# Kernel tuning notes

Measured on AMD Instinct MI355X. Metric: run time of the kernel, lower is better.

## Reference

```python
import jax, jax.numpy as jnp
import numpy as np

NUM_T = 1000      # diffusion timesteps
TIME_DIM = 16     # gaussian time embedding size
DIST_DIM = 16     # gaussian distance embedding size


def _gsmear(x, stop, num_g):
    # GaussianSmearing with linearly spaced centers in [0, stop]
    offsets = jnp.linspace(0.0, stop, num_g)
    coeff = -0.5 / (offsets[1] - offsets[0]) ** 2
    return jnp.exp(coeff * (x[:, None] - offsets[None, :]) ** 2)


def setup_inputs():
    key = jax.random.key(0)
    ks = jax.random.split(key, 20)
    N, EH, G = 20000, 100000, 1000          # nodes, halfedges, graphs
    NT, ND, ED, L, NE = 16, 256, 128, 2, 5   # node types, node_dim, edge_dim, blocks, edge types
    h_node = jax.nn.one_hot(jax.random.randint(ks[0], (N,), 0, NT), NT, dtype=jnp.float32)
    pos_node = jax.random.normal(ks[1], (N, 3), dtype=jnp.float32) * 3.0
    batch_node = jnp.sort(jax.random.randint(ks[2], (N,), 0, G))
    half = jax.random.randint(ks[3], (2, EH), 0, N)
    edge_index = jnp.concatenate([half, half[::-1]], axis=1)  # halfedges + flipped
    bh = jnp.sort(jax.random.randint(ks[4], (EH,), 0, G))
    batch_edge = jnp.concatenate([bh, bh], axis=0)
    t = jax.random.randint(ks[5], (G,), 0, NUM_T)

    def w(k, shape):
        fan_in = shape[-2] if len(shape) > 1 else shape[-1]
        return jax.random.normal(k, shape, dtype=jnp.float32) / np.sqrt(fan_in)

    e_in = ED + 2 * ND + DIST_DIM + 1
    return {
        'h_node': h_node, 'pos_node': pos_node, 'batch_node': batch_node,
        'edge_index': edge_index, 'batch_edge': batch_edge, 't': t,
        'W_node_emb': w(ks[6], (NT, ND - TIME_DIM)),
        'W_edge_emb': w(ks[7], (2 * NT, ED - TIME_DIM)),
        'We1': w(ks[8], (L, e_in, ED)), 'be1': jnp.zeros((L, ED), jnp.float32),
        'We2': w(ks[9], (L, ED, ED)), 'be2': jnp.zeros((L, ED), jnp.float32),
        'Wm': w(ks[10], (L, ND + ED, ND)), 'bm': jnp.zeros((L, ND), jnp.float32),
        'Wn1': w(ks[11], (L, 2 * ND + 1, ND)), 'bn1': jnp.zeros((L, ND), jnp.float32),
        'Wn2': w(ks[12], (L, ND, ND)), 'bn2': jnp.zeros((L, ND), jnp.float32),
        'Wd1': w(ks[13], (ED + ND, ED)), 'bd1': jnp.zeros((ED,), jnp.float32),
        'Wd2': w(ks[14], (ED, ED)), 'bd2': jnp.zeros((ED,), jnp.float32),
        'Wd3': w(ks[15], (ED, NE)), 'bd3': jnp.zeros((NE,), jnp.float32),
    }


def reference(h_node, pos_node, batch_node, edge_index, batch_edge, t,
              W_node_emb, W_edge_emb, We1, be1, We2, be2, Wm, bm,
              Wn1, bn1, Wn2, bn2, Wd1, bd1, Wd2, bd2, Wd3, bd3):
    src, dst = edge_index[0], edge_index[1]
    N = h_node.shape[0]
    L = We1.shape[0]

    # edge input features: concat of endpoint node features (gather)
    h_e0 = jnp.concatenate([h_node[src], h_node[dst]], axis=-1)

    tn = t[batch_node].astype(jnp.float32)  # per-node timestep
    te = t[batch_edge].astype(jnp.float32)  # per-edge timestep
    # linear embed + gaussian-smeared time embedding
    h_n = jnp.concatenate([h_node @ W_node_emb, _gsmear(tn, float(NUM_T), TIME_DIM)], axis=-1)
    h_e = jnp.concatenate([h_e0 @ W_edge_emb, _gsmear(te, float(NUM_T), TIME_DIM)], axis=-1)
    node_time = (tn / NUM_T)[:, None]
    edge_time = (te / NUM_T)[:, None]

    # geometric edge features
    d = jnp.linalg.norm(pos_node[dst] - pos_node[src], axis=-1)
    dist_emb = _gsmear(d, 10.0, DIST_DIM)

    # NodeEdgeNet: alternating edge / node residual updates
    for l in range(L):
        e_in = jnp.concatenate([h_e, h_n[src], h_n[dst], dist_emb, edge_time], axis=-1)
        h_e = h_e + jax.nn.relu(e_in @ We1[l] + be1[l]) @ We2[l] + be2[l]
        msg = jax.nn.relu(jnp.concatenate([h_n[src], h_e], axis=-1) @ Wm[l] + bm[l])
        agg = jax.ops.segment_sum(msg, dst, num_segments=N)
        n_in = jnp.concatenate([h_n, agg, node_time], axis=-1)
        h_n = h_n + jax.nn.relu(n_in @ Wn1[l] + bn1[l]) @ Wn2[l] + bn2[l]

    # symmetrize halfedges and decode edge types
    nh = h_e.shape[0] // 2
    h_ext = jnp.concatenate([h_e[:nh] + h_e[nh:],
                             h_n[src[:nh]] + h_n[dst[:nh]]], axis=-1)
    h = jax.nn.relu(h_ext @ Wd1 + bd1)
    h = jax.nn.relu(h @ Wd2 + bd2)
    return h @ Wd3 + bd3
```

## Files before the change

kernel.cpp:

```cpp
#include <hip/hip_runtime.h>
#include <math.h>


typedef __attribute__((ext_vector_type(8)))  short bf16x8;
typedef __attribute__((ext_vector_type(16))) float f32x16;

__device__ __forceinline__ float b2f(unsigned short u) {
    union { float f; unsigned int i; } x; x.i = ((unsigned int)u) << 16; return x.f;
}
__device__ __forceinline__ unsigned short f2b(float f) {
    union { float f; unsigned int i; } x; x.f = f;
    unsigned int r = x.i + 0x7fffu + ((x.i >> 16) & 1u);
    return (unsigned short)(r >> 16);
}
__device__ __forceinline__ bf16x8 ld8(const unsigned short* p) { return *(const bf16x8*)p; }
__device__ __forceinline__ bf16x8 zero8() { bf16x8 r = {0,0,0,0,0,0,0,0}; return r; }
__device__ __forceinline__ bf16x8 add8(bf16x8 a, bf16x8 b) {
    bf16x8 r;
#pragma unroll
    for (int j = 0; j < 8; j++) r[j] = (short)f2b(b2f((unsigned short)a[j]) + b2f((unsigned short)b[j]));
    return r;
}

#define MFMA4(ACC, A0, A1, B0, B1)                                                   \
    ACC[0][0] = __builtin_amdgcn_mfma_f32_32x32x16_bf16(A0, B0, ACC[0][0], 0, 0, 0); \
    ACC[0][1] = __builtin_amdgcn_mfma_f32_32x32x16_bf16(A0, B1, ACC[0][1], 0, 0, 0); \
    ACC[1][0] = __builtin_amdgcn_mfma_f32_32x32x16_bf16(A1, B0, ACC[1][0], 0, 0, 0); \
    ACC[1][1] = __builtin_amdgcn_mfma_f32_32x32x16_bf16(A1, B1, ACC[1][1], 0, 0, 0);

#define LANE_SETUP()                                  \
    const int tid  = threadIdx.x;                     \
    const int lane = tid & 63;                        \
    const int wave = tid >> 6;                        \
    const int wm = wave >> 1, wn = wave & 1;          \
    const int l31 = lane & 31, l5 = lane >> 5;        \
    (void)wm; (void)wn; (void)lane;

#define PIPELINE4(NITER, FETCH, ACC)                                  \
    {                                                                 \
        bf16x8 pa0[2], pb0[2], pa1[2], pb1[2], pa2[2], pb2[2];        \
        FETCH(0, pa0, pb0);                                           \
        if (1 < (NITER)) FETCH(1, pa1, pb1);                          \
        _Pragma("unroll")                                             \
        for (int i = 0; i < (NITER); i++) {                           \
            if (i + 2 < (NITER)) FETCH(i + 2, pa2, pb2);              \
            MFMA4(ACC, pa0[0], pa0[1], pb0[0], pb0[1]);               \
            pa0[0] = pa1[0]; pa0[1] = pa1[1];                         \
            pb0[0] = pb1[0]; pb0[1] = pb1[1];                         \
            pa1[0] = pa2[0]; pa1[1] = pa2[1];                         \
            pb1[0] = pb2[0]; pb1[1] = pb2[1];                         \
        }                                                             \
    }

#define PIPELINE2(NITER, FETCH, ACC)                                  \
    {                                                                 \
        bf16x8 pa0, pb0[2], pa1, pb1[2], pa2, pb2[2];                 \
        FETCH(0, pa0, pb0);                                           \
        if (1 < (NITER)) FETCH(1, pa1, pb1);                          \
        _Pragma("unroll")                                             \
        for (int i = 0; i < (NITER); i++) {                           \
            if (i + 2 < (NITER)) FETCH(i + 2, pa2, pb2);              \
            ACC[0] = __builtin_amdgcn_mfma_f32_32x32x16_bf16(pa0, pb0[0], ACC[0], 0, 0, 0); \
            ACC[1] = __builtin_amdgcn_mfma_f32_32x32x16_bf16(pa0, pb0[1], ACC[1], 0, 0, 0); \
            pa0 = pa1; pb0[0] = pb1[0]; pb0[1] = pb1[1];              \
            pa1 = pa2; pb1[0] = pb2[0]; pb1[1] = pb2[1];              \
        }                                                             \
    }

__global__ void zero_i32_k(int* p, int n) {
    int i = blockIdx.x * 256 + threadIdx.x;
    if (i < n) p[i] = 0;
}
__global__ void hist_k(const int* __restrict__ dst, int* __restrict__ cnt, int E) {
    int e = blockIdx.x * 256 + threadIdx.x;
    if (e < E) atomicAdd(&cnt[dst[e]], 1);
}
__global__ __launch_bounds__(256) void scan_k(int* __restrict__ cnt, int N) {
    __shared__ int s[256];
    const int tidx  = threadIdx.x;
    const int chunk = (N + 255) / 256;
    const int lo = tidx * chunk;
    const int hi = (lo + chunk < N) ? lo + chunk : N;
    int sum = 0;
    for (int i = lo; i < hi; i++) sum += cnt[i];
    s[tidx] = sum;
    __syncthreads();
    for (int d = 1; d < 256; d <<= 1) {
        int t = (tidx >= d) ? s[tidx - d] : 0;
        __syncthreads();
        s[tidx] += t;
        __syncthreads();
    }
    int base = s[tidx] - sum;
    for (int i = lo; i < hi; i++) {
        int c = cnt[i];
        cnt[i] = base;
        base += c;
    }
}
__global__ void fill_k(const int* __restrict__ src, const int* __restrict__ dst,
                       const int* __restrict__ batch_edge, int* __restrict__ cur,
                       int* __restrict__ eids, int* __restrict__ pos,
                       int* __restrict__ srcp, int* __restrict__ dstp,
                       int* __restrict__ bep, int E) {
    int e = blockIdx.x * 256 + threadIdx.x;
    if (e < E) {
        int p = atomicAdd(&cur[dst[e]], 1);
        eids[p] = e;
        pos[e]  = p;
        srcp[p] = src[e];
        dstp[p] = dst[e];
        bep[p]  = batch_edge[e];
    }
}
__global__ void pad_k(int* eids, int* srcp, int* dstp, int* bep, int E, int Epad) {
    int i = E + blockIdx.x * 256 + threadIdx.x;
    if (i < Epad) { eids[i] = -1; srcp[i] = 0; dstp[i] = -1; bep[i] = 0; }
}

// ... 39 lines not shown
            int col = seg * 8 + j;
            float dx = x - (1000.0f / 15.0f) * (float)(col - 240);
            v[j] = (short)f2b(expf(-1.125e-4f * dx * dx));
        }
    }
    *(bf16x8*)&h_n[(size_t)row * 256 + seg * 8] = v;
}

__global__ void embed_edge_k(const int* __restrict__ typ,
                             const float* __restrict__ We,
                             const int* __restrict__ srcp,
                             const int* __restrict__ dstp,
                             const int* __restrict__ bep,
                             const int* __restrict__ t,
                             unsigned short* __restrict__ h_e, int E) {
    int idx = blockIdx.x * 256 + threadIdx.x;
    if (idx >= E * 16) return;
    int row = idx >> 4, seg = idx & 15;
    bf16x8 v;
    if (seg < 14) {
        int d0 = dstp[row]; if (d0 < 0) d0 = 0;
        const float* ws = We + (size_t)typ[srcp[row]] * 112 + seg * 8;
        const float* wd = We + (size_t)(16 + typ[d0]) * 112 + seg * 8;
#pragma unroll
        for (int j = 0; j < 8; j++) v[j] = (short)f2b(ws[j] + wd[j]);
    } else {
        float x = (float)t[bep[row]];
#pragma unroll
        for (int j = 0; j < 8; j++) {
            int col = seg * 8 + j;
            float dx = x - (1000.0f / 15.0f) * (float)(col - 112);
            v[j] = (short)f2b(expf(-1.125e-4f * dx * dx));
        }
    }
    *(bf16x8*)&h_e[(size_t)row * 128 + seg * 8] = v;
}

__global__ __launch_bounds__(256) void edge_fused_k(
    unsigned short* __restrict__ h_e, const unsigned short* __restrict__ h_n,
    const unsigned short* __restrict__ Wt1, const float* __restrict__ be1,
    const unsigned short* __restrict__ Wt2, const float* __restrict__ be2,
    const float* __restrict__ pos, const int* __restrict__ srcp,
    const int* __restrict__ dstp, const int* __restrict__ t,
    const int* __restrict__ bep, int E)
{
    __shared__ __align__(16) char smem[128 * 136 * 2];
    unsigned short (*As)[8][8] = (unsigned short(*)[8][8])smem;
    unsigned short (*Bs)[8][8] = (unsigned short(*)[8][8])(smem + 16384);
    unsigned short (*H)[136]   = (unsigned short(*)[136])smem;

    LANE_SETUP();
    const int row0 = blockIdx.x * 128;
    const int srow = tid >> 3, sks = tid & 7;

    int rge[4], sg[4], dg[4]; bool okr[4];
#pragma unroll
    for (int p = 0; p < 4; p++) {
        int r = row0 + srow + p * 32;
        okr[p] = r < E;
        rge[p] = okr[p] ? r : 0;
        sg[p]  = srcp[rge[p]];
        dg[p]  = dstp[rge[p]]; if (dg[p] < 0) dg[p] = 0;
    }

    f32x16 acc[2][2] = {};
    for (int kc = 0; kc < 11; kc++) {
        const int cg = kc * 8 + sks;
#pragma unroll
        for (int p = 0; p < 4; p++) {
            int row = srow + p * 32;
            bf16x8 v;
            if (!okr[p] || cg >= 83) {
                v = zero8();
            } else if (cg < 16) {
                v = ld8(h_e + (size_t)rge[p] * 128 + (cg << 3));
            } else if (cg < 48) {
                v = ld8(h_n + (size_t)sg[p] * 256 + ((cg - 16) << 3));
            } else if (cg < 80) {
                v = ld8(h_n + (size_t)dg[p] * 256 + ((cg - 48) << 3));
            } else if (cg < 82) {
                float dx = pos[dg[p] * 3 + 0] - pos[sg[p] * 3 + 0];
                float dy = pos[dg[p] * 3 + 1] - pos[sg[p] * 3 + 1];
                float dz = pos[dg[p] * 3 + 2] - pos[sg[p] * 3 + 2];
                float dist = sqrtf(dx * dx + dy * dy + dz * dz);
#pragma unroll
                for (int j = 0; j < 8; j++) {
                    float u = dist - (10.0f / 15.0f) * (float)((cg - 80) * 8 + j);
                    v[j] = (short)f2b(expf(-1.125f * u * u));
                }
            } else {
                v = zero8();
                v[0] = (short)f2b((float)t[bep[rge[p]]] * 1e-3f);
            }
            *(bf16x8*)&As[row][sks ^ (row & 7)][0] = v;
        }
#pragma unroll
        for (int p = 0; p < 4; p++) {
            int col = srow + p * 32;
            bf16x8 v = (cg < 84) ? ld8(Wt1 + (size_t)col * 672 + (cg << 3)) : zero8();
            *(bf16x8*)&Bs[col][sks ^ (col & 7)][0] = v;
        }
        __syncthreads();
#pragma unroll
        for (int s = 0; s < 4; s++) {
            const int ks  = s * 2 + l5;
            const int ra0 = wm * 64 + l31, ra1 = ra0 + 32;
            const int ca0 = wn * 64 + l31, ca1 = ca0 + 32;
            bf16x8 a0 = *(const bf16x8*)&As[ra0][ks ^ (ra0 & 7)][0];
            bf16x8 a1 = *(const bf16x8*)&As[ra1][ks ^ (ra1 & 7)][0];
            bf16x8 b0 = *(const bf16x8*)&Bs[ca0][ks ^ (ca0 & 7)][0];
            bf16x8 b1 = *(const bf16x8*)&Bs[ca1][ks ^ (ca1 & 7)][0];
            MFMA4(acc, a0, a1, b0, b1);
        }
        __syncthreads();
    }

#pragma unroll
    for (int mt = 0; mt < 2; mt++)
#pragma unroll
        for (int nt = 0; nt < 2; nt++)
#pragma unroll
            for (int r = 0; r < 16; r++) {
                int lrow = wm * 64 + mt * 32 + (r & 3) + 8 * (r >> 2) + 4 * l5;
                int col  = wn * 64 + nt * 32 + l31;
                float v = acc[mt][nt][r] + be1[col];
                H[lrow][col] = f2b(fmaxf(v, 0.f));
            }
    __syncthreads();

    const unsigned short* W2a = Wt2 + (size_t)(wn * 64 + l31) * 128;
    const unsigned short* W2b = Wt2 + (size_t)(wn * 64 + 32 + l31) * 128;
    f32x16 acc2[2][2] = {};
#define EF2_FETCH(i, A, B)                                          \
    {                                                               \
        const int c = 2 * (i) + l5;                                 \
        A[0] = *(const bf16x8*)&H[wm * 64 + l31][c << 3];           \
        A[1] = *(const bf16x8*)&H[wm * 64 + 32 + l31][c << 3];      \
        B[0] = ld8(W2a + (c << 3));                                 \
        B[1] = ld8(W2b + (c << 3));                                 \
    }
    PIPELINE4(8, EF2_FETCH, acc2)
#undef EF2_FETCH

#pragma unroll
    for (int mt = 0; mt < 2; mt++)
#pragma unroll
        for (int nt = 0; nt < 2; nt++)
#pragma unroll
            for (int r = 0; r < 16; r++) {
                int lrow = wm * 64 + mt * 32 + (r & 3) + 8 * (r >> 2) + 4 * l5;
                int grow = row0 + lrow;
                if (grow >= E) continue;
                int col = wn * 64 + nt * 32 + l31;
                size_t off = (size_t)grow * 128 + col;
                float v = acc2[mt][nt][r] + be2[col] + b2f(h_e[off]);
                h_e[off] = f2b(v);
            }
}

__global__ __launch_bounds__(256) void msg_k(
    const unsigned short* __restrict__ h_e, const unsigned short* __restrict__ h_n,
    const unsigned short* __restrict__ Wtm, const float* __restrict__ bm,
    const int* __restrict__ srcp, const int* __restrict__ dstp,
    float* __restrict__ agg, int E, int nRowTiles)
{
    __shared__ __align__(16) char smem[33024 + 512];
    unsigned short (*As)[8][8] = (unsigned short(*)[8][8])smem;
    unsigned short (*Bs)[8][8] = (unsigned short(*)[8][8])(smem + 16384);
    float (*T)[129] = (float(*)[129])smem;
    int* dstv = (int*)(smem + 33024);

    LANE_SETUP();
    const int b    = blockIdx.x;
    const int rowt = (b >> 4) * 8 + (b & 7);
    const int colh = (b >> 3) & 1;
    if (rowt >= nRowTiles) return;
    const int row0 = rowt * 128;
    const int col0 = colh * 128;

    if (tid < 128) dstv[tid] = dstp[row0 + tid];

    const int srow = tid >> 3, sks = tid & 7;

    f32x16 acc[2][2] = {};
    for (int kc = 0; kc < 6; kc++) {
        const int cg = kc * 8 + sks;
#pragma unroll
        for (int p = 0; p < 4; p++) {
            int row = srow + p * 32;
            int r   = row0 + row;
            bf16x8 v;
            if (r < E) {
                if (cg < 32) v = ld8(h_n + (size_t)srcp[r] * 256 + (cg << 3));
                else         v = ld8(h_e + (size_t)r * 128 + ((cg - 32) << 3));
            } else v = zero8();
            *(bf16x8*)&As[row][sks ^ (row & 7)][0] = v;
        }
#pragma unroll
        for (int p = 0; p < 4; p++) {
            int col = srow + p * 32;
            bf16x8 v = ld8(Wtm + (size_t)(col0 + col) * 384 + (cg << 3));
            *(bf16x8*)&Bs[col][sks ^ (col & 7)][0] = v;
        }
        __syncthreads();
#pragma unroll
        for (int s = 0; s < 4; s++) {
            const int ks  = s * 2 + l5;
            const int ra0 = wm * 64 + l31, ra1 = ra0 + 32;
            const int ca0 = wn * 64 + l31, ca1 = ca0 + 32;
            bf16x8 a0 = *(const bf16x8*)&As[ra0][ks ^ (ra0 & 7)][0];
            bf16x8 a1 = *(const bf16x8*)&As[ra1][ks ^ (ra1 & 7)][0];
            bf16x8 b0 = *(const bf16x8*)&Bs[ca0][ks ^ (ca0 & 7)][0];
            bf16x8 b1 = *(const bf16x8*)&Bs[ca1][ks ^ (ca1 & 7)][0];
            MFMA4(acc, a0, a1, b0, b1);
        }
        __syncthreads();
    }

    for (int ph = 0; ph < 2; ph++) {
        __syncthreads();
        if (wm == ph) {
#pragma unroll
            for (int mt = 0; mt < 2; mt++)
#pragma unroll
                for (int nt = 0; nt < 2; nt++)
#pragma unroll
                    for (int r = 0; r < 16; r++) {
                        int lrow = mt * 32 + (r & 3) + 8 * (r >> 2) + 4 * l5;
                        int col  = wn * 64 + nt * 32 + l31;
                        T[lrow][col] = acc[mt][nt][r] + bm[col0 + col];
                    }
        }
        __syncthreads();
        const int col = tid & 127, seg = tid >> 7;
        const int gcol = col0 + col;
        float run = 0.f; int prev = -1;
#pragma unroll 4
        for (int i = 0; i < 32; i++) {
            int lr = seg * 32 + i;
            int d  = dstv[ph * 64 + lr];
            float v = fmaxf(T[lr][col], 0.f);
            if (d != prev) {
                if (prev >= 0 && run != 0.f) atomicAdd(&agg[(size_t)prev * 256 + gcol], run);
                run = 0.f; prev = d;
            }
            if (d >= 0) run += v;
        }
        if (prev >= 0 && run != 0.f) atomicAdd(&agg[(size_t)prev * 256 + gcol], run);
    }
}

__global__ __launch_bounds__(256) void nin_k(
    const unsigned short* __restrict__ h_n, const float* __restrict__ agg,
    const unsigned short* __restrict__ Wtn1, const float* __restrict__ bn1,
    const int* __restrict__ batch_node, const int* __restrict__ t,
    unsigned short* __restrict__ Hn, int N)
{
    LANE_SETUP();
    const int row0 = blockIdx.x * 64;
    const int col0 = blockIdx.y * 128;

    int rr = row0 + wm * 32 + l31;
    bool ok = rr < N;
    int r = ok ? rr : 0;
    float timev = (float)t[batch_node[r]] * 1e-3f;
    const unsigned short* hp = h_n + (size_t)r * 256;
    const float*          ap = agg + (size_t)r * 256;

    const unsigned short* Wa = Wtn1 + (size_t)(col0 + wn * 64 + l31) * 544;
    const unsigned short* Wb = Wtn1 + (size_t)(col0 + wn * 64 + 32 + l31) * 544;

    f32x16 acc[2] = {};
#define NIN_FETCH(i, A, B)                                              \
    {                                                                   \
        const int c = 2 * (i) + l5;                                     \
        if (!ok) A = zero8();                                           \
        else if (c < 32) A = ld8(hp + (c << 3));                        \
        else if (c < 64) {                                              \
            const float* q = ap + ((c - 32) << 3);                      \
            bf16x8 v;                                                   \
            _Pragma("unroll")                                           \
            for (int j = 0; j < 8; j++) v[j] = (short)f2b(q[j]);        \
            A = v;                                                      \
        } else if (c == 64) { A = zero8(); A[0] = (short)f2b(timev); }  \
        else A = zero8();                                               \
        B[0] = ld8(Wa + (c << 3));                                      \
        B[1] = ld8(Wb + (c << 3));                                      \
    }
    PIPELINE2(34, NIN_FETCH, acc)
#undef NIN_FETCH

#pragma unroll
    for (int nt = 0; nt < 2; nt++)
#pragma unroll
        for (int r2 = 0; r2 < 16; r2++) {
            int lrow = wm * 32 + (r2 & 3) + 8 * (r2 >> 2) + 4 * l5;
            int grow = row0 + lrow;
            if (grow >= N) continue;
            int col = col0 + wn * 64 + nt * 32 + l31;
            float v = fmaxf(acc[nt][r2] + bn1[col], 0.f);
            Hn[(size_t)grow * 256 + col] = f2b(v);
        }
}

__global__ __launch_bounds__(256) void node_plain_k(
    const unsigned short* __restrict__ Hn, const unsigned short* __restrict__ Wtn2,
    const float* __restrict__ bn2, unsigned short* __restrict__ h_n, int N)
{
    LANE_SETUP();
    const int row0 = blockIdx.x * 64;
    const int col0 = blockIdx.y * 128;

    int rr = row0 + wm * 32 + l31;
    bool ok = rr < N;
    const unsigned short* hp = Hn + (size_t)(ok ? rr : 0) * 256;

    const unsigned short* Wa = Wtn2 + (size_t)(col0 + wn * 64 + l31) * 256;
    const unsigned short* Wb = Wtn2 + (size_t)(col0 + wn * 64 + 32 + l31) * 256;

    f32x16 acc[2] = {};
#define NP_FETCH(i, A, B)                          \
    {                                              \
        const int c = 2 * (i) + l5;                \
        A = ok ? ld8(hp + (c << 3)) : zero8();     \
        B[0] = ld8(Wa + (c << 3));                 \
        B[1] = ld8(Wb + (c << 3));                 \
    }
    PIPELINE2(16, NP_FETCH, acc)
#undef NP_FETCH

#pragma unroll
    for (int nt = 0; nt < 2; nt++)
#pragma unroll
        for (int r2 = 0; r2 < 16; r2++) {
            int lrow = wm * 32 + (r2 & 3) + 8 * (r2 >> 2) + 4 * l5;
            int grow = row0 + lrow;
            if (grow >= N) continue;
            int col = col0 + wn * 64 + nt * 32 + l31;
            size_t off = (size_t)grow * 256 + col;
            float v = acc[nt][r2] + bn2[col] + b2f(h_n[off]);
            h_n[off] = f2b(v);
        }
}

__global__ __launch_bounds__(256) void dec_fused_k(
    const unsigned short* __restrict__ h_e, const unsigned short* __restrict__ h_n,
    const unsigned short* __restrict__ Wtd1, const float* __restrict__ bd1,
    const unsigned short* __restrict__ Wtd2, const float* __restrict__ bd2,
    const float* __restrict__ Wd3, const float* __restrict__ bd3,
    const int* __restrict__ src, const int* __restrict__ dst,
    const int* __restrict__ pos, float* __restrict__ out, int nh)
{
    __shared__ __align__(16) char smem[128 * 136 * 2];
    __shared__ __align__(16) unsigned short H2[128][136];
    unsigned short (*As)[8][8] = (unsigned short(*)[8][8])smem;
    unsigned short (*Bs)[8][8] = (unsigned short(*)[8][8])(smem + 16384);
    unsigned short (*H1)[136]  = (unsigned short(*)[136])smem;

    LANE_SETUP();
    const int row0 = blockIdx.x * 128;
    const int srow = tid >> 3, sks = tid & 7;

    const unsigned short *pe1[4], *pe2[4], *pns[4], *pnd[4]; bool okr[4];
#pragma unroll
    for (int p = 0; p < 4; p++) {
        int r = row0 + srow + p * 32;
        okr[p] = r < nh;
        int rg = okr[p] ? r : 0;
        pe1[p] = h_e + (size_t)pos[rg] * 128;
        pe2[p] = h_e + (size_t)pos[rg + nh] * 128;
        pns[p] = h_n + (size_t)src[rg] * 256;
        pnd[p] = h_n + (size_t)dst[rg] * 256;
    }

    f32x16 acc[2][2] = {};
    for (int kc = 0; kc < 6; kc++) {
        const int cg = kc * 8 + sks;
#pragma unroll
        for (int p = 0; p < 4; p++) {
            int row = srow + p * 32;
            bf16x8 v;
            if (!okr[p]) v = zero8();
            else if (cg < 16) v = add8(ld8(pe1[p] + (cg << 3)), ld8(pe2[p] + (cg << 3)));
            else              v = add8(ld8(pns[p] + ((cg - 16) << 3)), ld8(pnd[p] + ((cg - 16) << 3)));
            *(bf16x8*)&As[row][sks ^ (row & 7)][0] = v;
        }
#pragma unroll
        for (int p = 0; p < 4; p++) {
            int col = srow + p * 32;
            bf16x8 v = ld8(Wtd1 + (size_t)col * 384 + (cg << 3));
            *(bf16x8*)&Bs[col][sks ^ (col & 7)][0] = v;
        }
        __syncthreads();
#pragma unroll
        for (int s = 0; s < 4; s++) {
            const int ks  = s * 2 + l5;
            const int ra0 = wm * 64 + l31, ra1 = ra0 + 32;
            const int ca0 = wn * 64 + l31, ca1 = ca0 + 32;
            bf16x8 a0 = *(const bf16x8*)&As[ra0][ks ^ (ra0 & 7)][0];
            bf16x8 a1 = *(const bf16x8*)&As[ra1][ks ^ (ra1 & 7)][0];
            bf16x8 b0 = *(const bf16x8*)&Bs[ca0][ks ^ (ca0 & 7)][0];
            bf16x8 b1 = *(const bf16x8*)&Bs[ca1][ks ^ (ca1 & 7)][0];
            MFMA4(acc, a0, a1, b0, b1);
        }
        __syncthreads();
    }

#pragma unroll
    for (int mt = 0; mt < 2; mt++)
#pragma unroll
        for (int nt = 0; nt < 2; nt++)
#pragma unroll
            for (int r = 0; r < 16; r++) {
                int lrow = wm * 64 + mt * 32 + (r & 3) + 8 * (r >> 2) + 4 * l5;
                int col  = wn * 64 + nt * 32 + l31;
                H1[lrow][col] = f2b(fmaxf(acc[mt][nt][r] + bd1[col], 0.f));
            }
    __syncthreads();

    const unsigned short* W2a = Wtd2 + (size_t)(wn * 64 + l31) * 128;
    const unsigned short* W2b = Wtd2 + (size_t)(wn * 64 + 32 + l31) * 128;
    f32x16 acc2[2][2] = {};
#define DC2_FETCH(i, A, B)                                          \
    {                                                               \
        const int c = 2 * (i) + l5;                                 \
        A[0] = *(const bf16x8*)&H1[wm * 64 + l31][c << 3];          \
        A[1] = *(const bf16x8*)&H1[wm * 64 + 32 + l31][c << 3];     \
        B[0] = ld8(W2a + (c << 3));                                 \
        B[1] = ld8(W2b + (c << 3));                                 \
    }
    PIPELINE4(8, DC2_FETCH, acc2)
#undef DC2_FETCH

#pragma unroll
    for (int mt = 0; mt < 2; mt++)
#pragma unroll
        for (int nt = 0; nt < 2; nt++)
#pragma unroll
            for (int r = 0; r < 16; r++) {
                int lrow = wm * 64 + mt * 32 + (r & 3) + 8 * (r >> 2) + 4 * l5;
                int col  = wn * 64 + nt * 32 + l31;
                H2[lrow][col] = f2b(fmaxf(acc2[mt][nt][r] + bd2[col], 0.f));
            }
    __syncthreads();

    if (tid < 128) {
        int grow = row0 + tid;
        if (grow < nh) {
            float a5[5] = {0.f, 0.f, 0.f, 0.f, 0.f};
            for (int ks = 0; ks < 16; ks++) {
                bf16x8 hv = *(const bf16x8*)&H2[tid][ks << 3];
#pragma unroll
                for (int j = 0; j < 8; j++) {
                    float a = b2f((unsigned short)hv[j]);
                    int   k = ks * 8 + j;
#pragma unroll
                    for (int c5 = 0; c5 < 5; c5++) a5[c5] += a * Wd3[k * 5 + c5];
                }
            }
#pragma unroll
            for (int c5 = 0; c5 < 5; c5++) out[(size_t)grow * 5 + c5] = a5[c5] + bd3[c5];
        }
    }
}


__global__ void zero_k(float* p, long n) {
    long i = (long)blockIdx.x * 256 + threadIdx.x;
    if (i < n) p[i] = 0.f;
}


extern "C" void kernel_launch(void* const* d_in, const int* in_sizes, int n_in,
                              void* d_out, int out_size, void* d_ws, size_t ws_size,
                              hipStream_t stream) {
    const float* h_node     = (const float*)d_in[0];
    const float* pos_node   = (const float*)d_in[1];
    const int*   batch_node = (const int*)d_in[2];
    const int*   edge_index = (const int*)d_in[3];
    const int*   batch_edge = (const int*)d_in[4];
    const int*   t          = (const int*)d_in[5];
    const float* W_node_emb = (const float*)d_in[6];
    const float* W_edge_emb = (const float*)d_in[7];
    const float* We1 = (const float*)d_in[8];
    const float* be1 = (const float*)d_in[9];
    const float* We2 = (const float*)d_in[10];
    const float* be2 = (const float*)d_in[11];
    const float* Wm  = (const float*)d_in[12];
    const float* bm  = (const float*)d_in[13];
    const float* Wn1 = (const float*)d_in[14];
    const float* bn1 = (const float*)d_in[15];
    const float* Wn2 = (const float*)d_in[16];
    const float* bn2 = (const float*)d_in[17];
    const float* Wd1 = (const float*)d_in[18];
    const float* bd1 = (const float*)d_in[19];
    const float* Wd2 = (const float*)d_in[20];
    const float* bd2 = (const float*)d_in[21];
    const float* Wd3 = (const float*)d_in[22];
    const float* bd3 = (const float*)d_in[23];

    const int N  = in_sizes[0] / 16;
    const int E  = in_sizes[3] / 2;
    const int nh = E / 2;
    const int* src = edge_index;
    const int* dst = edge_index + E;

    const int gE   = (E + 127) / 128;
    const int gE8  = ((gE + 7) / 8) * 8;
    const int gN64 = (N + 63) / 64;
    const int Epad = gE * 128;

    float* agg  = (float*)d_ws;
    int*   cnt  = (int*)(agg + (size_t)N * 256);
    int*   eids = cnt + N;
    int*   pos  = eids + Epad;
    int*   srcp = pos + Epad;
    int*   dstp = srcp + Epad;
    int*   bep  = dstp + Epad;
    int*   typ  = bep + Epad;
    unsigned short* h_e = (unsigned short*)(typ + N);
    unsigned short* h_n = h_e + (size_t)E * 128;
    unsigned short* Hn  = h_n + (size_t)N * 256;
    unsigned short* Wt1  = Hn + (size_t)N * 256;
    unsigned short* Wt2  = Wt1 + 2 * 128 * 672;
    unsigned short* Wtm  = Wt2 + 2 * 128 * 128;
    unsigned short* Wtn1 = Wtm + 2 * 256 * 384;
    unsigned short* Wtn2 = Wtn1 + 2 * 256 * 544;
    unsigned short* Wtd1 = Wtn2 + 2 * 256 * 256;
    unsigned short* Wtd2 = Wtd1 + 128 * 384;

    zero_i32_k<<<(N + 255) / 256, 256, 0, stream>>>(cnt, N);
    hist_k<<<(E + 255) / 256, 256, 0, stream>>>(dst, cnt, E);
    scan_k<<<1, 256, 0, stream>>>(cnt, N);
    fill_k<<<(E + 255) / 256, 256, 0, stream>>>(src, dst, batch_edge, cnt,
                                                eids, pos, srcp, dstp, bep, E);
    if (Epad > E) pad_k<<<1, 256, 0, stream>>>(eids, srcp, dstp, bep, E, Epad);
    typ_k<<<(N + 255) / 256, 256, 0, stream>>>(h_node, typ, N);

    TrAll ta;
    for (int l = 0; l < 2; l++) {
        ta.d[l * 5 + 0] = { We1 + (size_t)l * 657 * 128, Wt1 + (size_t)l * 128 * 672, 657, 128, 672 };
        ta.d[l * 5 + 1] = { We2 + (size_t)l * 128 * 128, Wt2 + (size_t)l * 128 * 128, 128, 128, 128 };
        ta.d[l * 5 + 2] = { Wm  + (size_t)l * 384 * 256, Wtm + (size_t)l * 256 * 384, 384, 256, 384 };
        ta.d[l * 5 + 3] = { Wn1 + (size_t)l * 513 * 256, Wtn1 + (size_t)l * 256 * 544, 513, 256, 544 };
        ta.d[l * 5 + 4] = { Wn2 + (size_t)l * 256 * 256, Wtn2 + (size_t)l * 256 * 256, 256, 256, 256 };
    }
    ta.d[10] = { Wd1, Wtd1, 384, 128, 384 };
    ta.d[11] = { Wd2, Wtd2, 128, 128, 128 };
    tr_all_k<<<dim3(48, 12), 256, 0, stream>>>(ta);

    embed_node_k<<<(N * 32 + 255) / 256, 256, 0, stream>>>(typ, W_node_emb, batch_node, t, h_n, N);
    embed_edge_k<<<(E * 16 + 255) / 256, 256, 0, stream>>>(typ, W_edge_emb, srcp, dstp, bep, t, h_e, E);

    for (int l = 0; l < 2; l++) {
        edge_fused_k<<<gE, 256, 0, stream>>>(
            h_e, h_n, Wt1 + (size_t)l * 128 * 672, be1 + l * 128,
            Wt2 + (size_t)l * 128 * 128, be2 + l * 128,
            pos_node, srcp, dstp, t, bep, E);

        zero_k<<<(int)(((long)N * 256 + 255) / 256), 256, 0, stream>>>(agg, (long)N * 256);
        msg_k<<<gE8 * 2, 256, 0, stream>>>(
            h_e, h_n, Wtm + (size_t)l * 256 * 384, bm + l * 256, srcp, dstp, agg, E, gE);

        nin_k<<<dim3(gN64, 2), 256, 0, stream>>>(
            h_n, agg, Wtn1 + (size_t)l * 256 * 544, bn1 + l * 256, batch_node, t, Hn, N);

        node_plain_k<<<dim3(gN64, 2), 256, 0, stream>>>(
            Hn, Wtn2 + (size_t)l * 256 * 256, bn2 + l * 256, h_n, N);
    }

    dec_fused_k<<<(nh + 127) / 128, 256, 0, stream>>>(
        h_e, h_n, Wtd1, bd1, Wtd2, bd2, Wd3, bd3, src, dst, pos, (float*)d_out, nh);
}
```

Baseline: 962.0 us.

## Compute full msg width per block and LDS-tile node GEMMs at 128 rows

msg_k now computes both 128-column halves of the 256-wide message output in one block, so the gathered A tile (h_n[src] and h_e rows) is loaded once instead of twice, at the cost of more LDS (48KB) and twice the accumulator registers. nin_k and node_plain_k drop their direct-from-global register-pipelined MFMA loops and switch to 128x128 LDS-staged tiles with swizzled shared memory, matching the edge kernels. This halves the node grid and shares A/B tiles across waves, but adds block-wide barriers, and the higher register and LDS use may reduce occupancy.

```diff
diff --git a/kernel.cpp b/kernel.cpp
--- a/kernel.cpp
+++ b/kernel.cpp
@@ -49,21 +49,6 @@
             pb0[0] = pb1[0]; pb0[1] = pb1[1];                         \
             pa1[0] = pa2[0]; pa1[1] = pa2[1];                         \
             pb1[0] = pb2[0]; pb1[1] = pb2[1];                         \
-        }                                                             \
-    }
-
-#define PIPELINE2(NITER, FETCH, ACC)                                  \
-    {                                                                 \
-        bf16x8 pa0, pb0[2], pa1, pb1[2], pa2, pb2[2];                 \
-        FETCH(0, pa0, pb0);                                           \
-        if (1 < (NITER)) FETCH(1, pa1, pb1);                          \
-        _Pragma("unroll")                                             \
-        for (int i = 0; i < (NITER); i++) {                           \
-            if (i + 2 < (NITER)) FETCH(i + 2, pa2, pb2);              \
-            ACC[0] = __builtin_amdgcn_mfma_f32_32x32x16_bf16(pa0, pb0[0], ACC[0], 0, 0, 0); \
-            ACC[1] = __builtin_amdgcn_mfma_f32_32x32x16_bf16(pa0, pb0[1], ACC[1], 0, 0, 0); \
-            pa0 = pa1; pb0[0] = pb1[0]; pb0[1] = pb1[1];              \
-            pa1 = pa2; pb1[0] = pb2[0]; pb1[1] = pb2[1];              \
         }                                                             \
     }
 
@@ -320,27 +305,23 @@
     const unsigned short* __restrict__ h_e, const unsigned short* __restrict__ h_n,
     const unsigned short* __restrict__ Wtm, const float* __restrict__ bm,
     const int* __restrict__ srcp, const int* __restrict__ dstp,
-    float* __restrict__ agg, int E, int nRowTiles)
+    float* __restrict__ agg, int E)
 {
-    __shared__ __align__(16) char smem[33024 + 512];
-    unsigned short (*As)[8][8] = (unsigned short(*)[8][8])smem;
-    unsigned short (*Bs)[8][8] = (unsigned short(*)[8][8])(smem + 16384);
+    __shared__ __align__(16) char smem[49152 + 512];
+    unsigned short (*As)[8][8]  = (unsigned short(*)[8][8])smem;
+    unsigned short (*Bs0)[8][8] = (unsigned short(*)[8][8])(smem + 16384);
+    unsigned short (*Bs1)[8][8] = (unsigned short(*)[8][8])(smem + 32768);
     float (*T)[129] = (float(*)[129])smem;
-    int* dstv = (int*)(smem + 33024);
+    int* dstv = (int*)(smem + 49152);
 
     LANE_SETUP();
-    const int b    = blockIdx.x;
-    const int rowt = (b >> 4) * 8 + (b & 7);
-    const int colh = (b >> 3) & 1;
-    if (rowt >= nRowTiles) return;
-    const int row0 = rowt * 128;
-    const int col0 = colh * 128;
+    const int row0 = blockIdx.x * 128;
 
     if (tid < 128) dstv[tid] = dstp[row0 + tid];
 
     const int srow = tid >> 3, sks = tid & 7;
 
-    f32x16 acc[2][2] = {};
+    f32x16 acc[2][2][2] = {};
     for (int kc = 0; kc < 6; kc++) {
         const int cg = kc * 8 + sks;
 #pragma unroll
@@ -357,7 +338,109 @@
 #pragma unroll
         for (int p = 0; p < 4; p++) {
             int col = srow + p * 32;
-            bf16x8 v = ld8(Wtm + (size_t)(col0 + col) * 384 + (cg << 3));
+            bf16x8 v0 = ld8(Wtm + (size_t)col * 384 + (cg << 3));
+            bf16x8 v1 = ld8(Wtm + (size_t)(128 + col) * 384 + (cg << 3));
+            *(bf16x8*)&Bs0[col][sks ^ (col & 7)][0] = v0;
+            *(bf16x8*)&Bs1[col][sks ^ (col & 7)][0] = v1;
+        }
+        __syncthreads();
+#pragma unroll
+        for (int s = 0; s < 4; s++) {
+            const int ks  = s * 2 + l5;
+            const int ra0 = wm * 64 + l31, ra1 = ra0 + 32;
+            const int ca0 = wn * 64 + l31, ca1 = ca0 + 32;
+            bf16x8 a0  = *(const bf16x8*)&As[ra0][ks ^ (ra0 & 7)][0];
+            bf16x8 a1  = *(const bf16x8*)&As[ra1][ks ^ (ra1 & 7)][0];
+            bf16x8 b00 = *(const bf16x8*)&Bs0[ca0][ks ^ (ca0 & 7)][0];
+            bf16x8 b01 = *(const bf16x8*)&Bs0[ca1][ks ^ (ca1 & 7)][0];
+            bf16x8 b10 = *(const bf16x8*)&Bs1[ca0][ks ^ (ca0 & 7)][0];
+            bf16x8 b11 = *(const bf16x8*)&Bs1[ca1][ks ^ (ca1 & 7)][0];
+            MFMA4(acc[0], a0, a1, b00, b01);
+            MFMA4(acc[1], a0, a1, b10, b11);
+        }
+        __syncthreads();
+    }
+
+    for (int ch = 0; ch < 2; ch++) {
+        const int col0 = ch * 128;
+        for (int ph = 0; ph < 2; ph++) {
+            __syncthreads();
+            if (wm == ph) {
+#pragma unroll
+                for (int mt = 0; mt < 2; mt++)
+#pragma unroll
+                    for (int nt = 0; nt < 2; nt++)
+#pragma unroll
+                        for (int r = 0; r < 16; r++) {
+                            int lrow = mt * 32 + (r & 3) + 8 * (r >> 2) + 4 * l5;
+                            int col  = wn * 64 + nt * 32 + l31;
+                            T[lrow][col] = acc[ch][mt][nt][r] + bm[col0 + col];
+                        }
+            }
+            __syncthreads();
+            const int col = tid & 127, seg = tid >> 7;
+            const int gcol = col0 + col;
+            float run = 0.f; int prev = -1;
+#pragma unroll 4
+            for (int i = 0; i < 32; i++) {
+                int lr = seg * 32 + i;
+                int d  = dstv[ph * 64 + lr];
+                float v = fmaxf(T[lr][col], 0.f);
+                if (d != prev) {
+                    if (prev >= 0 && run != 0.f) atomicAdd(&agg[(size_t)prev * 256 + gcol], run);
+                    run = 0.f; prev = d;
+                }
+                if (d >= 0) run += v;
+            }
+            if (prev >= 0 && run != 0.f) atomicAdd(&agg[(size_t)prev * 256 + gcol], run);
+        }
+    }
+}
+
+__global__ __launch_bounds__(256) void nin_k(
+    const unsigned short* __restrict__ h_n, const float* __restrict__ agg,
+    const unsigned short* __restrict__ Wtn1, const float* __restrict__ bn1,
+    const int* __restrict__ batch_node, const int* __restrict__ t,
+    unsigned short* __restrict__ Hn, int N)
+{
+    __shared__ __align__(16) char smem[32768];
+    unsigned short (*As)[8][8] = (unsigned short(*)[8][8])smem;
+    unsigned short (*Bs)[8][8] = (unsigned short(*)[8][8])(smem + 16384);
+
+    LANE_SETUP();
+    const int row0 = blockIdx.x * 128;
+    const int col0 = blockIdx.y * 128;
+    const int srow = tid >> 3, sks = tid & 7;
+
+    int rg[4]; bool okr[4]; float tv[4];
+#pragma unroll
+    for (int p = 0; p < 4; p++) {
+        int r = row0 + srow + p * 32;
+        okr[p] = r < N;
+        rg[p]  = okr[p] ? r : 0;
+        tv[p]  = (float)t[batch_node[rg[p]]] * 1e-3f;
+    }
+
+    f32x16 acc[2][2] = {};
+    for (int kc = 0; kc < 9; kc++) {
+        const int cg = kc * 8 + sks;
+#pragma unroll
+        for (int p = 0; p < 4; p++) {
+            int row = srow + p * 32;
+            bf16x8 v;
+            if (!okr[p] || cg > 64) v = zero8();
+            else if (cg < 32) v = ld8(h_n + (size_t)rg[p] * 256 + (cg << 3));
+            else if (cg < 64) {
+                const float* q = agg + (size_t)rg[p] * 256 + ((cg - 32) << 3);
+#pragma unroll
+                for (int j = 0; j < 8; j++) v[j] = (short)f2b(q[j]);
+            } else { v = zero8(); v[0] = (short)f2b(tv[p]); }
+            *(bf16x8*)&As[row][sks ^ (row & 7)][0] = v;
+        }
+#pragma unroll
+        for (int p = 0; p < 4; p++) {
+            int col = srow + p * 32;
+            bf16x8 v = (cg < 68) ? ld8(Wtn1 + (size_t)(col0 + col) * 544 + (cg << 3)) : zero8();
             *(bf16x8*)&Bs[col][sks ^ (col & 7)][0] = v;
         }
         __syncthreads();
@@ -375,130 +458,79 @@
         __syncthreads();
     }
 
-    for (int ph = 0; ph < 2; ph++) {
-        __syncthreads();
-        if (wm == ph) {
-#pragma unroll
-            for (int mt = 0; mt < 2; mt++)
-#pragma unroll
-                for (int nt = 0; nt < 2; nt++)
-#pragma unroll
-                    for (int r = 0; r < 16; r++) {
-                        int lrow = mt * 32 + (r & 3) + 8 * (r >> 2) + 4 * l5;
-                        int col  = wn * 64 + nt * 32 + l31;
-                        T[lrow][col] = acc[mt][nt][r] + bm[col0 + col];
-                    }
-        }
-        __syncthreads();
-        const int col = tid & 127, seg = tid >> 7;
-        const int gcol = col0 + col;
-        float run = 0.f; int prev = -1;
-#pragma unroll 4
-        for (int i = 0; i < 32; i++) {
-            int lr = seg * 32 + i;
-            int d  = dstv[ph * 64 + lr];
-            float v = fmaxf(T[lr][col], 0.f);
-            if (d != prev) {
-                if (prev >= 0 && run != 0.f) atomicAdd(&agg[(size_t)prev * 256 + gcol], run);
-                run = 0.f; prev = d;
-            }
-            if (d >= 0) run += v;
-        }
-        if (prev >= 0 && run != 0.f) atomicAdd(&agg[(size_t)prev * 256 + gcol], run);
-    }
-}
-
-__global__ __launch_bounds__(256) void nin_k(
-    const unsigned short* __restrict__ h_n, const float* __restrict__ agg,
-    const unsigned short* __restrict__ Wtn1, const float* __restrict__ bn1,
-    const int* __restrict__ batch_node, const int* __restrict__ t,
-    unsigned short* __restrict__ Hn, int N)
-{
-    LANE_SETUP();
-    const int row0 = blockIdx.x * 64;
-    const int col0 = blockIdx.y * 128;
-
-    int rr = row0 + wm * 32 + l31;
-    bool ok = rr < N;
-    int r = ok ? rr : 0;
-    float timev = (float)t[batch_node[r]] * 1e-3f;
-    const unsigned short* hp = h_n + (size_t)r * 256;
-    const float*          ap = agg + (size_t)r * 256;
-
-    const unsigned short* Wa = Wtn1 + (size_t)(col0 + wn * 64 + l31) * 544;
-    const unsigned short* Wb = Wtn1 + (size_t)(col0 + wn * 64 + 32 + l31) * 544;
-
-    f32x16 acc[2] = {};
-#define NIN_FETCH(i, A, B)                                              \
-    {                                                                   \
-        const int c = 2 * (i) + l5;                                     \
-        if (!ok) A = zero8();                                           \
-        else if (c < 32) A = ld8(hp + (c << 3));                        \
-        else if (c < 64) {                                              \
-            const float* q = ap + ((c - 32) << 3);                      \
-            bf16x8 v;                                                   \
-            _Pragma("unroll")                                           \
-            for (int j = 0; j < 8; j++) v[j] = (short)f2b(q[j]);        \
-            A = v;                                                      \
-        } else if (c == 64) { A = zero8(); A[0] = (short)f2b(timev); }  \
-        else A = zero8();                                               \
-        B[0] = ld8(Wa + (c << 3));                                      \
-        B[1] = ld8(Wb + (c << 3));                                      \
-    }
-    PIPELINE2(34, NIN_FETCH, acc)
-#undef NIN_FETCH
-
-#pragma unroll
-    for (int nt = 0; nt < 2; nt++)
-#pragma unroll
-        for (int r2 = 0; r2 < 16; r2++) {
-            int lrow = wm * 32 + (r2 & 3) + 8 * (r2 >> 2) + 4 * l5;
-            int grow = row0 + lrow;
-            if (grow >= N) continue;
-            int col = col0 + wn * 64 + nt * 32 + l31;
-            float v = fmaxf(acc[nt][r2] + bn1[col], 0.f);
-            Hn[(size_t)grow * 256 + col] = f2b(v);
-        }
+#pragma unroll
+    for (int mt = 0; mt < 2; mt++)
+#pragma unroll
+        for (int nt = 0; nt < 2; nt++)
+#pragma unroll
+            for (int r = 0; r < 16; r++) {
+                int lrow = wm * 64 + mt * 32 + (r & 3) + 8 * (r >> 2) + 4 * l5;
+                int grow = row0 + lrow;
+                if (grow >= N) continue;
+                int col = col0 + wn * 64 + nt * 32 + l31;
+                float v = fmaxf(acc[mt][nt][r] + bn1[col], 0.f);
+                Hn[(size_t)grow * 256 + col] = f2b(v);
+            }
 }
 
 __global__ __launch_bounds__(256) void node_plain_k(
     const unsigned short* __restrict__ Hn, const unsigned short* __restrict__ Wtn2,
     const float* __restrict__ bn2, unsigned short* __restrict__ h_n, int N)
 {
+    __shared__ __align__(16) char smem[32768];
+    unsigned short (*As)[8][8] = (unsigned short(*)[8][8])smem;
+    unsigned short (*Bs)[8][8] = (unsigned short(*)[8][8])(smem + 16384);
+
     LANE_SETUP();
-    const int row0 = blockIdx.x * 64;
+    const int row0 = blockIdx.x * 128;
     const int col0 = blockIdx.y * 128;
-
-    int rr = row0 + wm * 32 + l31;
-    bool ok = rr < N;
-    const unsigned short* hp = Hn + (size_t)(ok ? rr : 0) * 256;
-
-    const unsigned short* Wa = Wtn2 + (size_t)(col0 + wn * 64 + l31) * 256;
-    const unsigned short* Wb = Wtn2 + (size_t)(col0 + wn * 64 + 32 + l31) * 256;
-
-    f32x16 acc[2] = {};
-#define NP_FETCH(i, A, B)                          \
-    {                                              \
-        const int c = 2 * (i) + l5;                \
-        A = ok ? ld8(hp + (c << 3)) : zero8();     \
-        B[0] = ld8(Wa + (c << 3));                 \
-        B[1] = ld8(Wb + (c << 3));                 \
-    }
-    PIPELINE2(16, NP_FETCH, acc)
-#undef NP_FETCH
-
-#pragma unroll
-    for (int nt = 0; nt < 2; nt++)
-#pragma unroll
-        for (int r2 = 0; r2 < 16; r2++) {
-            int lrow = wm * 32 + (r2 & 3) + 8 * (r2 >> 2) + 4 * l5;
-            int grow = row0 + lrow;
-            if (grow >= N) continue;
-            int col = col0 + wn * 64 + nt * 32 + l31;
-            size_t off = (size_t)grow * 256 + col;
-            float v = acc[nt][r2] + bn2[col] + b2f(h_n[off]);
-            h_n[off] = f2b(v);
-        }
+    const int srow = tid >> 3, sks = tid & 7;
+
+    f32x16 acc[2][2] = {};
+    for (int kc = 0; kc < 4; kc++) {
+        const int cg = kc * 8 + sks;
+#pragma unroll
+        for (int p = 0; p < 4; p++) {
+            int row = srow + p * 32;
+            int r   = row0 + row;
+            bf16x8 v = (r < N) ? ld8(Hn + (size_t)r * 256 + (cg << 3)) : zero8();
+            *(bf16x8*)&As[row][sks ^ (row & 7)][0] = v;
+        }
+#pragma unroll
+        for (int p = 0; p < 4; p++) {
+            int col = srow + p * 32;
+            bf16x8 v = ld8(Wtn2 + (size_t)(col0 + col) * 256 + (cg << 3));
+            *(bf16x8*)&Bs[col][sks ^ (col & 7)][0] = v;
+        }
+        __syncthreads();
+#pragma unroll
+        for (int s = 0; s < 4; s++) {
+            const int ks  = s * 2 + l5;
+            const int ra0 = wm * 64 + l31, ra1 = ra0 + 32;
+            const int ca0 = wn * 64 + l31, ca1 = ca0 + 32;
+            bf16x8 a0 = *(const bf16x8*)&As[ra0][ks ^ (ra0 & 7)][0];
+            bf16x8 a1 = *(const bf16x8*)&As[ra1][ks ^ (ra1 & 7)][0];
+            bf16x8 b0 = *(const bf16x8*)&Bs[ca0][ks ^ (ca0 & 7)][0];
+            bf16x8 b1 = *(const bf16x8*)&Bs[ca1][ks ^ (ca1 & 7)][0];
+            MFMA4(acc, a0, a1, b0, b1);
+        }
+        __syncthreads();
+    }
+
+#pragma unroll
+    for (int mt = 0; mt < 2; mt++)
+#pragma unroll
+        for (int nt = 0; nt < 2; nt++)
+#pragma unroll
+            for (int r = 0; r < 16; r++) {
+                int lrow = wm * 64 + mt * 32 + (r & 3) + 8 * (r >> 2) + 4 * l5;
+                int grow = row0 + lrow;
+                if (grow >= N) continue;
+                int col = col0 + wn * 64 + nt * 32 + l31;
+                size_t off = (size_t)grow * 256 + col;
+                float v = acc[mt][nt][r] + bn2[col] + b2f(h_n[off]);
+                h_n[off] = f2b(v);
+            }
 }
 
 __global__ __launch_bounds__(256) void dec_fused_k(
@@ -663,10 +695,9 @@
     const int* src = edge_index;
     const int* dst = edge_index + E;
 
-    const int gE   = (E + 127) / 128;
-    const int gE8  = ((gE + 7) / 8) * 8;
-    const int gN64 = (N + 63) / 64;
-    const int Epad = gE * 128;
+    const int gE    = (E + 127) / 128;
+    const int gN128 = (N + 127) / 128;
+    const int Epad  = gE * 128;
 
     float* agg  = (float*)d_ws;
     int*   cnt  = (int*)(agg + (size_t)N * 256);
@@ -717,13 +748,13 @@
             pos_node, srcp, dstp, t, bep, E);
 
         zero_k<<<(int)(((long)N * 256 + 255) / 256), 256, 0, stream>>>(agg, (long)N * 256);
-        msg_k<<<gE8 * 2, 256, 0, stream>>>(
-            h_e, h_n, Wtm + (size_t)l * 256 * 384, bm + l * 256, srcp, dstp, agg, E, gE);
-
-        nin_k<<<dim3(gN64, 2), 256, 0, stream>>>(
+        msg_k<<<gE, 256, 0, stream>>>(
+            h_e, h_n, Wtm + (size_t)l * 256 * 384, bm + l * 256, srcp, dstp, agg, E);
+
+        nin_k<<<dim3(gN128, 2), 256, 0, stream>>>(
             h_n, agg, Wtn1 + (size_t)l * 256 * 544, bn1 + l * 256, batch_node, t, Hn, N);
 
-        node_plain_k<<<dim3(gN64, 2), 256, 0, stream>>>(
+        node_plain_k<<<dim3(gN128, 2), 256, 0, stream>>>(
             Hn, Wtn2 + (size_t)l * 256 * 256, bn2 + l * 256, h_n, N);
     }
 
```

After: 1.035 ms. 7.6% more time.

## Prefetch next K-chunk into registers during MFMA compute in GEMM kernels

Applied to the files above, without the earlier changes.

The first-stage GEMM loops in the edge, message and decoder kernels now use register double buffering. Each iteration writes the already-fetched A/B tiles to LDS, then issues the global gathers for the next K-chunk before the barrier and MFMA compute, so gather latency overlaps with compute. The cost is extra VGPRs for the pA/pB/qA/qB staging arrays, which may reduce occupancy. Row pointers in the message kernel are also hoisted out of the loop.

```diff
diff --git a/kernel.cpp b/kernel.cpp
--- a/kernel.cpp
+++ b/kernel.cpp
@@ -65,6 +65,19 @@
             pa0 = pa1; pb0[0] = pb1[0]; pb0[1] = pb1[1];              \
             pa1 = pa2; pb1[0] = pb2[0]; pb1[1] = pb2[1];              \
         }                                                             \
+    }
+
+#define STAGED_COMPUTE(As, Bs, ACC)                                         \
+    _Pragma("unroll")                                                       \
+    for (int s = 0; s < 4; s++) {                                           \
+        const int ks  = s * 2 + l5;                                         \
+        const int ra0 = wm * 64 + l31, ra1 = ra0 + 32;                      \
+        const int ca0 = wn * 64 + l31, ca1 = ca0 + 32;                      \
+        bf16x8 a0 = *(const bf16x8*)&As[ra0][ks ^ (ra0 & 7)][0];            \
+        bf16x8 a1 = *(const bf16x8*)&As[ra1][ks ^ (ra1 & 7)][0];            \
+        bf16x8 b0 = *(const bf16x8*)&Bs[ca0][ks ^ (ca0 & 7)][0];            \
+        bf16x8 b1 = *(const bf16x8*)&Bs[ca1][ks ^ (ca1 & 7)][0];            \
+        MFMA4(ACC, a0, a1, b0, b1);                                         \
     }
 
 __global__ void zero_i32_k(int* p, int n) {
@@ -210,6 +223,7 @@
     LANE_SETUP();
     const int row0 = blockIdx.x * 128;
     const int srow = tid >> 3, sks = tid & 7;
+    const int sx   = sks ^ (srow & 7);
 
     int rge[4], sg[4], dg[4]; bool okr[4];
 #pragma unroll
@@ -221,57 +235,65 @@
         dg[p]  = dstp[rge[p]]; if (dg[p] < 0) dg[p] = 0;
     }
 
+#define EF_LOADA(KC, A)                                                        \
+    {                                                                          \
+        const int cg = (KC) * 8 + sks;                                         \
+        _Pragma("unroll")                                                      \
+        for (int p = 0; p < 4; p++) {                                          \
+            bf16x8 v;                                                          \
+            if (!okr[p] || cg >= 83) {                                         \
+                v = zero8();                                                   \
+            } else if (cg < 16) {                                              \
+                v = ld8(h_e + (size_t)rge[p] * 128 + (cg << 3));               \
+            } else if (cg < 48) {                                              \
+                v = ld8(h_n + (size_t)sg[p] * 256 + ((cg - 16) << 3));         \
+            } else if (cg < 80) {                                              \
+                v = ld8(h_n + (size_t)dg[p] * 256 + ((cg - 48) << 3));         \
+            } else if (cg < 82) {                                              \
+                float dx = pos[dg[p] * 3 + 0] - pos[sg[p] * 3 + 0];            \
+                float dy = pos[dg[p] * 3 + 1] - pos[sg[p] * 3 + 1];            \
+                float dz = pos[dg[p] * 3 + 2] - pos[sg[p] * 3 + 2];            \
+                float dist = sqrtf(dx * dx + dy * dy + dz * dz);               \
+                _Pragma("unroll")                                              \
+                for (int j = 0; j < 8; j++) {                                  \
+                    float u = dist - (10.0f / 15.0f) * (float)((cg - 80) * 8 + j); \
+                    v[j] = (short)f2b(expf(-1.125f * u * u));                  \
+                }                                                              \
+            } else {                                                           \
+                v = zero8();                                                   \
+                v[0] = (short)f2b((float)t[bep[rge[p]]] * 1e-3f);              \
+            }                                                                  \
+            A[p] = v;                                                          \
+        }                                                                      \
+    }
+#define EF_LOADB(KC, B)                                                        \
+    {                                                                          \
+        const int cg = (KC) * 8 + sks;                                         \
+        _Pragma("unroll")                                                      \
+        for (int p = 0; p < 4; p++) {                                          \
+            int col = srow + p * 32;                                           \
+            B[p] = (cg < 84) ? ld8(Wt1 + (size_t)col * 672 + (cg << 3)) : zero8(); \
+        }                                                                      \
+    }
+
     f32x16 acc[2][2] = {};
+    bf16x8 pA[4], pB[4], qA[4], qB[4];
+    EF_LOADA(0, pA); EF_LOADB(0, pB);
     for (int kc = 0; kc < 11; kc++) {
-        const int cg = kc * 8 + sks;
 #pragma unroll
         for (int p = 0; p < 4; p++) {
-            int row = srow + p * 32;
-            bf16x8 v;
-            if (!okr[p] || cg >= 83) {
-                v = zero8();
-            } else if (cg < 16) {
-                v = ld8(h_e + (size_t)rge[p] * 128 + (cg << 3));
-            } else if (cg < 48) {
-                v = ld8(h_n + (size_t)sg[p] * 256 + ((cg - 16) << 3));
-            } else if (cg < 80) {
-                v = ld8(h_n + (size_t)dg[p] * 256 + ((cg - 48) << 3));
-            } else if (cg < 82) {
-                float dx = pos[dg[p] * 3 + 0] - pos[sg[p] * 3 + 0];
-                float dy = pos[dg[p] * 3 + 1] - pos[sg[p] * 3 + 1];
-                float dz = pos[dg[p] * 3 + 2] - pos[sg[p] * 3 + 2];
-                float dist = sqrtf(dx * dx + dy * dy + dz * dz);
-#pragma unroll
-                for (int j = 0; j < 8; j++) {
-                    float u = dist - (10.0f / 15.0f) * (float)((cg - 80) * 8 + j);
-                    v[j] = (short)f2b(expf(-1.125f * u * u));
-                }
-            } else {
-                v = zero8();
-                v[0] = (short)f2b((float)t[bep[rge[p]]] * 1e-3f);
-            }
-            *(bf16x8*)&As[row][sks ^ (row & 7)][0] = v;
-        }
-#pragma unroll
-        for (int p = 0; p < 4; p++) {
-            int col = srow + p * 32;
-            bf16x8 v = (cg < 84) ? ld8(Wt1 + (size_t)col * 672 + (cg << 3)) : zero8();
-            *(bf16x8*)&Bs[col][sks ^ (col & 7)][0] = v;
-        }
-        __syncthreads();
-#pragma unroll
-        for (int s = 0; s < 4; s++) {
-            const int ks  = s * 2 + l5;
-            const int ra0 = wm * 64 + l31, ra1 = ra0 + 32;
-            const int ca0 = wn * 64 + l31, ca1 = ca0 + 32;
-            bf16x8 a0 = *(const bf16x8*)&As[ra0][ks ^ (ra0 & 7)][0];
-            bf16x8 a1 = *(const bf16x8*)&As[ra1][ks ^ (ra1 & 7)][0];
-            bf16x8 b0 = *(const bf16x8*)&Bs[ca0][ks ^ (ca0 & 7)][0];
-            bf16x8 b1 = *(const bf16x8*)&Bs[ca1][ks ^ (ca1 & 7)][0];
-            MFMA4(acc, a0, a1, b0, b1);
-        }
-        __syncthreads();
-    }
+            *(bf16x8*)&As[srow + p * 32][sx][0] = pA[p];
+            *(bf16x8*)&Bs[srow + p * 32][sx][0] = pB[p];
+        }
+        if (kc + 1 < 11) { EF_LOADA(kc + 1, qA); EF_LOADB(kc + 1, qB); }
+        __syncthreads();
+        STAGED_COMPUTE(As, Bs, acc);
+        __syncthreads();
+#pragma unroll
+        for (int p = 0; p < 4; p++) { pA[p] = qA[p]; pB[p] = qB[p]; }
+    }
+#undef EF_LOADA
+#undef EF_LOADB
 
 #pragma unroll
     for (int mt = 0; mt < 2; mt++)
@@ -339,41 +361,56 @@
     if (tid < 128) dstv[tid] = dstp[row0 + tid];
 
     const int srow = tid >> 3, sks = tid & 7;
+    const int sx   = sks ^ (srow & 7);
+
+    const unsigned short *hns[4], *hep[4]; bool okr[4];
+#pragma unroll
+    for (int p = 0; p < 4; p++) {
+        int r = row0 + srow + p * 32;
+        okr[p] = r < E;
+        int rg = okr[p] ? r : 0;
+        hns[p] = h_n + (size_t)srcp[rg] * 256;
+        hep[p] = h_e + (size_t)rg * 128;
+    }
+
+#define MSG_LOADA(KC, A)                                                 \
+    {                                                                    \
+        const int cg = (KC) * 8 + sks;                                   \
+        _Pragma("unroll")                                                \
+        for (int p = 0; p < 4; p++) {                                    \
+            if (!okr[p])      A[p] = zero8();                            \
+            else if (cg < 32) A[p] = ld8(hns[p] + (cg << 3));            \
+            else              A[p] = ld8(hep[p] + ((cg - 32) << 3));     \
+        }                                                                \
+    }
+#define MSG_LOADB(KC, B)                                                 \
+    {                                                                    \
+        const int cg = (KC) * 8 + sks;                                   \
+        _Pragma("unroll")                                                \
+        for (int p = 0; p < 4; p++) {                                    \
+            int col = srow + p * 32;                                     \
+            B[p] = ld8(Wtm + (size_t)(col0 + col) * 384 + (cg << 3));    \
+        }                                                                \
+    }
 
     f32x16 acc[2][2] = {};
+    bf16x8 pA[4], pB[4], qA[4], qB[4];
+    MSG_LOADA(0, pA); MSG_LOADB(0, pB);
     for (int kc = 0; kc < 6; kc++) {
-        const int cg = kc * 8 + sks;
 #pragma unroll
         for (int p = 0; p < 4; p++) {
-            int row = srow + p * 32;
-            int r   = row0 + row;
-            bf16x8 v;
-            if (r < E) {
-                if (cg < 32) v = ld8(h_n + (size_t)srcp[r] * 256 + (cg << 3));
-                else         v = ld8(h_e + (size_t)r * 128 + ((cg - 32) << 3));
-            } else v = zero8();
-            *(bf16x8*)&As[row][sks ^ (row & 7)][0] = v;
-        }
-#pragma unroll
-        for (int p = 0; p < 4; p++) {
-            int col = srow + p * 32;
-            bf16x8 v = ld8(Wtm + (size_t)(col0 + col) * 384 + (cg << 3));
-            *(bf16x8*)&Bs[col][sks ^ (col & 7)][0] = v;
-        }
-        __syncthreads();
-#pragma unroll
-        for (int s = 0; s < 4; s++) {
-            const int ks  = s * 2 + l5;
-            const int ra0 = wm * 64 + l31, ra1 = ra0 + 32;
-            const int ca0 = wn * 64 + l31, ca1 = ca0 + 32;
-            bf16x8 a0 = *(const bf16x8*)&As[ra0][ks ^ (ra0 & 7)][0];
-            bf16x8 a1 = *(const bf16x8*)&As[ra1][ks ^ (ra1 & 7)][0];
-            bf16x8 b0 = *(const bf16x8*)&Bs[ca0][ks ^ (ca0 & 7)][0];
-            bf16x8 b1 = *(const bf16x8*)&Bs[ca1][ks ^ (ca1 & 7)][0];
-            MFMA4(acc, a0, a1, b0, b1);
-        }
-        __syncthreads();
-    }
+            *(bf16x8*)&As[srow + p * 32][sx][0] = pA[p];
+            *(bf16x8*)&Bs[srow + p * 32][sx][0] = pB[p];
+        }
+        if (kc + 1 < 6) { MSG_LOADA(kc + 1, qA); MSG_LOADB(kc + 1, qB); }
+        __syncthreads();
+        STAGED_COMPUTE(As, Bs, acc);
+        __syncthreads();
+#pragma unroll
+        for (int p = 0; p < 4; p++) { pA[p] = qA[p]; pB[p] = qB[p]; }
+    }
+#undef MSG_LOADA
+#undef MSG_LOADB
 
     for (int ph = 0; ph < 2; ph++) {
         __syncthreads();
@@ -518,6 +555,7 @@
     LANE_SETUP();
     const int row0 = blockIdx.x * 128;
     const int srow = tid >> 3, sks = tid & 7;
+    const int sx   = sks ^ (srow & 7);
 
     const unsigned short *pe1[4], *pe2[4], *pns[4], *pnd[4]; bool okr[4];
 #pragma unroll
@@ -531,38 +569,44 @@
         pnd[p] = h_n + (size_t)dst[rg] * 256;
     }
 
+#define DC_LOADA(KC, A)                                                              \
+    {                                                                                \
+        const int cg = (KC) * 8 + sks;                                               \
+        _Pragma("unroll")                                                            \
+        for (int p = 0; p < 4; p++) {                                                \
+            if (!okr[p])      A[p] = zero8();                                        \
+            else if (cg < 16) A[p] = add8(ld8(pe1[p] + (cg << 3)), ld8(pe2[p] + (cg << 3))); \
+            else              A[p] = add8(ld8(pns[p] + ((cg - 16) << 3)), ld8(pnd[p] + ((cg - 16) << 3))); \
+        }                                                                            \
+    }
+#define DC_LOADB(KC, B)                                                              \
+    {                                                                                \
+        const int cg = (KC) * 8 + sks;                                               \
+        _Pragma("unroll")                                                            \
+        for (int p = 0; p < 4; p++) {                                                \
+            int col = srow + p * 32;                                                 \
+            B[p] = ld8(Wtd1 + (size_t)col * 384 + (cg << 3));                        \
+        }                                                                            \
+    }
+
     f32x16 acc[2][2] = {};
+    bf16x8 pA[4], pB[4], qA[4], qB[4];
+    DC_LOADA(0, pA); DC_LOADB(0, pB);
     for (int kc = 0; kc < 6; kc++) {
-        const int cg = kc * 8 + sks;
 #pragma unroll
         for (int p = 0; p < 4; p++) {
-            int row = srow + p * 32;
-            bf16x8 v;
-            if (!okr[p]) v = zero8();
-            else if (cg < 16) v = add8(ld8(pe1[p] + (cg << 3)), ld8(pe2[p] + (cg << 3)));
-            else              v = add8(ld8(pns[p] + ((cg - 16) << 3)), ld8(pnd[p] + ((cg - 16) << 3)));
-            *(bf16x8*)&As[row][sks ^ (row & 7)][0] = v;
-        }
-#pragma unroll
-        for (int p = 0; p < 4; p++) {
-            int col = srow + p * 32;
-            bf16x8 v = ld8(Wtd1 + (size_t)col * 384 + (cg << 3));
-            *(bf16x8*)&Bs[col][sks ^ (col & 7)][0] = v;
-        }
-        __syncthreads();
-#pragma unroll
-        for (int s = 0; s < 4; s++) {
-            const int ks  = s * 2 + l5;
-            const int ra0 = wm * 64 + l31, ra1 = ra0 + 32;
-            const int ca0 = wn * 64 + l31, ca1 = ca0 + 32;
-            bf16x8 a0 = *(const bf16x8*)&As[ra0][ks ^ (ra0 & 7)][0];
-            bf16x8 a1 = *(const bf16x8*)&As[ra1][ks ^ (ra1 & 7)][0];
-            bf16x8 b0 = *(const bf16x8*)&Bs[ca0][ks ^ (ca0 & 7)][0];
-            bf16x8 b1 = *(const bf16x8*)&Bs[ca1][ks ^ (ca1 & 7)][0];
-            MFMA4(acc, a0, a1, b0, b1);
-        }
-        __syncthreads();
-    }
+            *(bf16x8*)&As[srow + p * 32][sx][0] = pA[p];
+            *(bf16x8*)&Bs[srow + p * 32][sx][0] = pB[p];
+        }
+        if (kc + 1 < 6) { DC_LOADA(kc + 1, qA); DC_LOADB(kc + 1, qB); }
+        __syncthreads();
+        STAGED_COMPUTE(As, Bs, acc);
+        __syncthreads();
+#pragma unroll
+        for (int p = 0; p < 4; p++) { pA[p] = qA[p]; pB[p] = qB[p]; }
+    }
+#undef DC_LOADA
+#undef DC_LOADB
 
 #pragma unroll
     for (int mt = 0; mt < 2; mt++)
```

Measured after the change: 866.5 us. -9.9%, faster.
